# Kernel tuning notes

Measured on AMD Instinct MI355X. Metric: run time of the kernel, lower is better.

The kernel has to match this reference:

```python
import jax, jax.numpy as jnp
import numpy as np

B, S, D_IN, D_QK, D_V = 4, 4096, 1024, 64, 64

def setup_inputs() -> dict:
    key = jax.random.key(0)
    ks = jax.random.split(key, 8)
    sd = 1.0 / np.sqrt(D_IN)
    return {
        "X": jax.random.normal(ks[0], (B, S, D_IN), dtype=jnp.float32),
        "mask": jnp.ones((B, S, 1), dtype=jnp.float32),
        "Wq": jax.random.uniform(ks[1], (D_IN, D_QK), jnp.float32, -sd, sd),
        "bq": jax.random.uniform(ks[2], (D_QK,), jnp.float32, -sd, sd),
        "Wk": jax.random.uniform(ks[3], (D_IN, D_QK), jnp.float32, -sd, sd),
        "bk": jax.random.uniform(ks[4], (D_QK,), jnp.float32, -sd, sd),
        "Wv": jax.random.uniform(ks[5], (D_IN, D_V), jnp.float32, -sd, sd),
        "bv": jax.random.uniform(ks[6], (D_V,), jnp.float32, -sd, sd),
    }

def reference(X, mask, Wq, bq, Wk, bk, Wv, bv):
    # ReLU-activated projections (no head split, no 1/sqrt(d) scaling)
    q = jax.nn.relu(jnp.einsum('bsd,df->bsf', X, Wq) + bq)   # [B,S,D_QK]
    k = jax.nn.relu(jnp.einsum('bsd,df->bsf', X, Wk) + bk)   # [B,S,D_QK]
    v = jax.nn.relu(jnp.einsum('bsd,df->bsf', X, Wv) + bv)   # [B,S,D_V]
    scores = jax.nn.softmax(jnp.einsum('bqf,bkf->bqk', q, k), axis=-1)  # [B,S,S]
    return jnp.einsum('bqk,bkf->bqf', scores, v) * mask       # mask applied AFTER AV
```

## Files before the change

kernel.cpp:

```cpp
#include <hip/hip_runtime.h>


typedef short s16x8 __attribute__((ext_vector_type(8)));
typedef float fx4   __attribute__((ext_vector_type(4)));
typedef unsigned short u16x4 __attribute__((ext_vector_type(4)));

#define LOG2E 1.4426950408889634f

__device__ __forceinline__ unsigned short f2bf(float x) {
    unsigned int u = __float_as_uint(x);
    u += 0x7FFFu + ((u >> 16) & 1u);
    return (unsigned short)(u >> 16);
}
__device__ __forceinline__ float bf2f(unsigned short b) {
    return __uint_as_float(((unsigned int)b) << 16);
}

__global__ __launch_bounds__(256) void prep_w_kernel(
    const float* __restrict__ Wq, const float* __restrict__ Wk, const float* __restrict__ Wv,
    unsigned short* __restrict__ wt_hi, unsigned short* __restrict__ wt_lo)
{
    __shared__ __align__(16) unsigned short sh[64][72];
    __shared__ __align__(16) unsigned short sl[64][72];

    const int y  = blockIdx.x;
    const int kt = blockIdx.y;
    const float* W = (y == 0) ? Wq : (y == 1) ? Wk : Wv;
    const int t  = threadIdx.x;

    const int kl = t >> 2;
    const int c0 = (t & 3) * 16;
    const float* src = W + (size_t)(kt * 64 + kl) * 64 + c0;
    #pragma unroll
    for (int j = 0; j < 4; j++) {
        fx4 v = *(const fx4*)(src + j * 4);
        #pragma unroll
        for (int i = 0; i < 4; i++) {
            float x = v[i];
            unsigned short h = f2bf(x);
            unsigned short l = f2bf(x - bf2f(h));
            sh[c0 + j * 4 + i][kl] = h;
            sl[c0 + j * 4 + i][kl] = l;
        }
    }
    __syncthreads();

    const int c  = t >> 2;
    const int k0 = (t & 3) * 16;
    size_t o = (size_t)(y * 64 + c) * 1024 + kt * 64 + k0;
    *(s16x8*)(wt_hi + o)     = *(const s16x8*)&sh[c][k0];
    *(s16x8*)(wt_hi + o + 8) = *(const s16x8*)&sh[c][k0 + 8];
    *(s16x8*)(wt_lo + o)     = *(const s16x8*)&sl[c][k0];
    *(s16x8*)(wt_lo + o + 8) = *(const s16x8*)&sl[c][k0 + 8];
}

__global__ __launch_bounds__(768, 3) void proj_kernel(
    const float* __restrict__ X,
    const unsigned short* __restrict__ wt_hi, const unsigned short* __restrict__ wt_lo,
    const float* __restrict__ bq, const float* __restrict__ bk, const float* __restrict__ bv,
    unsigned short* __restrict__ q_hi, unsigned short* __restrict__ q_lo,
    unsigned short* __restrict__ k_bf, unsigned short* __restrict__ vt_g)
{
    __shared__ __align__(16) unsigned short a_hi[64][72];
    __shared__ __align__(16) unsigned short a_lo[64][72];
    __shared__ __align__(16) unsigned short bsh[192][72];
    __shared__ __align__(16) unsigned short bsl[192][72];

    const int tid  = threadIdx.x;
    const int lane = tid & 63;
    const int w    = tid >> 6;
    const int quad = lane >> 4;
    const int l15  = lane & 15;
    const int rowg = w & 1;
    const int colg = w >> 1;
    const int y    = colg >> 1;
    const int ch   = colg & 1;

    const int m0 = blockIdx.x * 64;

    fx4 acc[2][2];
    #pragma unroll
    for (int i = 0; i < 2; i++)
        #pragma unroll
        for (int j = 0; j < 2; j++) acc[i][j] = (fx4){0.f, 0.f, 0.f, 0.f};

    const int xrow = tid >> 4;
    const int xoff = (tid & 15) * 4;
    const float* xb0 = X + (size_t)(m0 + xrow) * 1024 + xoff;
    const float* xb1 = X + (size_t)(m0 + xrow + 32) * 1024 + xoff;

    const int wrow = tid >> 2;
    const int wk   = (tid & 3) * 16;
    const size_t wb = (size_t)wrow * 1024 + wk;

    fx4   xr[4][2];
    s16x8 wrh[2][2], wrl[2][2];
    if (tid < 512) {
        #pragma unroll
        for (int d = 0; d < 4; d++) {
            xr[d][0] = *(const fx4*)(xb0 + d * 64);
            xr[d][1] = *(const fx4*)(xb1 + d * 64);
        }
    }
    #pragma unroll
    for (int d = 0; d < 2; d++) {
        wrh[d][0] = *(const s16x8*)(wt_hi + wb + d * 64);
        wrh[d][1] = *(const s16x8*)(wt_hi + wb + d * 64 + 8);
        wrl[d][0] = *(const s16x8*)(wt_lo + wb + d * 64);
        wrl[d][1] = *(const s16x8*)(wt_lo + wb + d * 64 + 8);
    }

    #pragma unroll 4
    for (int kc = 0; kc < 16; kc++) {
        if (kc) __syncthreads();
        if (tid < 512) {
            #pragma unroll
            for (int i = 0; i < 2; i++) {
                fx4 xv = xr[kc & 3][i];
                unsigned short h0 = f2bf(xv.x), h1 = f2bf(xv.y), h2 = f2bf(xv.z), h3 = f2bf(xv.w);
                unsigned short l0 = f2bf(xv.x - bf2f(h0)), l1 = f2bf(xv.y - bf2f(h1));
                unsigned short l2 = f2bf(xv.z - bf2f(h2)), l3 = f2bf(xv.w - bf2f(h3));
                *(u16x4*)&a_hi[xrow + i * 32][xoff] = (u16x4){h0, h1, h2, h3};
                *(u16x4*)&a_lo[xrow + i * 32][xoff] = (u16x4){l0, l1, l2, l3};
            }
        }
        *(s16x8*)&bsh[wrow][wk]     = wrh[kc & 1][0];
        *(s16x8*)&bsh[wrow][wk + 8] = wrh[kc & 1][1];
        *(s16x8*)&bsl[wrow][wk]     = wrl[kc & 1][0];
        *(s16x8*)&bsl[wrow][wk + 8] = wrl[kc & 1][1];
        __syncthreads();

        if (tid < 512 && kc < 12) {
            xr[kc & 3][0] = *(const fx4*)(xb0 + (kc + 4) * 64);
            xr[kc & 3][1] = *(const fx4*)(xb1 + (kc + 4) * 64);
        }
        if (kc < 14) {
            wrh[kc & 1][0] = *(const s16x8*)(wt_hi + wb + (kc + 2) * 64);
            wrh[kc & 1][1] = *(const s16x8*)(wt_hi + wb + (kc + 2) * 64 + 8);
            wrl[kc & 1][0] = *(const s16x8*)(wt_lo + wb + (kc + 2) * 64);
            wrl[kc & 1][1] = *(const s16x8*)(wt_lo + wb + (kc + 2) * 64 + 8);
        }

        s16x8 ah[2][2], al[2][2];
        #pragma unroll
        for (int sub = 0; sub < 2; sub++)
            #pragma unroll
            for (int ks = 0; ks < 2; ks++) {
                const int r = rowg * 32 + sub * 16 + l15;
                ah[sub][ks] = *(const s16x8*)&a_hi[r][ks * 32 + quad * 8];
                al[sub][ks] = *(const s16x8*)&a_lo[r][ks * 32 + quad * 8];
            }
        #pragma unroll
        for (int nt = 0; nt < 2; nt++) {
            const int br = colg * 32 + nt * 16 + l15;
            #pragma unroll
            for (int ks = 0; ks < 2; ks++) {
                s16x8 bh = *(const s16x8*)&bsh[br][ks * 32 + quad * 8];
                s16x8 bl = *(const s16x8*)&bsl[br][ks * 32 + quad * 8];
                #pragma unroll
                for (int sub = 0; sub < 2; sub++) {
                    acc[sub][nt] = __builtin_amdgcn_mfma_f32_16x16x32_bf16(ah[sub][ks], bh, acc[sub][nt], 0, 0, 0);
                    acc[sub][nt] = __builtin_amdgcn_mfma_f32_16x16x32_bf16(ah[sub][ks], bl, acc[sub][nt], 0, 0, 0);
                    acc[sub][nt] = __builtin_amdgcn_mfma_f32_16x16x32_bf16(al[sub][ks], bh, acc[sub][nt], 0, 0, 0);
                }
            }
        }
    }
    __syncthreads();

    const float* bias = (y == 0) ? bq : (y == 1) ? bk : bv;
    const int b   = m0 >> 12;
    const int s0b = m0 & 4095;
    unsigned short* vtr = &a_hi[0][0];

    #pragma unroll
    for (int sub = 0; sub < 2; sub++)
        #pragma unroll
        for (int nt = 0; nt < 2; nt++) {
            const int col = ch * 32 + nt * 16 + l15;
            const float bb = bias[col];
            const int rloc = rowg * 32 + sub * 16 + quad * 4;
            #pragma unroll
            for (int r = 0; r < 4; r++) {
                float v = fmaxf(acc[sub][nt][r] + bb, 0.f);
                size_t grow = (size_t)(m0 + rloc + r);
                if (y == 0) {
                    unsigned short h = f2bf(v);
                    unsigned short l = f2bf(v - bf2f(h));
                    q_hi[grow * 64 + col] = h;
                    q_lo[grow * 64 + col] = l;
                } else if (y == 1) {
                    k_bf[grow * 64 + col] = f2bf(v);
                } else {
                    vtr[col * 72 + rloc + r] = f2bf(v);
                }
            }
        }
    __syncthreads();
    if (tid < 512) {
        int row = tid >> 3;
        int off = (tid & 7) * 8;
        s16x8 vv = *(const s16x8*)&vtr[row * 72 + off];
        *(s16x8*)(vt_g + (size_t)(b * 64 + row) * 4096 + s0b + off) = vv;
    }
}

__global__ __launch_bounds__(512, 2) void attn_kernel(
    const unsigned short* __restrict__ q_hi, const unsigned short* __restrict__ q_lo,
    const unsigned short* __restrict__ k_bf, const unsigned short* __restrict__ vt_g,
    unsigned short* __restrict__ pOb, float* __restrict__ pL)
{
    __shared__ __align__(16) unsigned short kt[128][72];
    __shared__ __align__(16) unsigned short vt[64][136];
    __shared__ __align__(16) unsigned short pt[8][32][40];

    const int tid  = threadIdx.x;
    const int lane = tid & 63;
    const int w    = tid >> 6;
    const int quad = lane >> 4;
    const int l15  = lane & 15;
    const int ck   = blockIdx.y;
    const int b    = blockIdx.z;
    const int q0   = blockIdx.x * 256;

    const size_t qbase = ((size_t)b * 4096 + q0 + w * 32 + l15) * 64 + quad * 8;
    s16x8 qh[2][2], ql[2][2];
    #pragma unroll
    for (int sub = 0; sub < 2; sub++) {
        qh[sub][0] = *(const s16x8*)(q_hi + qbase + sub * 1024);
        qh[sub][1] = *(const s16x8*)(q_hi + qbase + sub * 1024 + 32);
        ql[sub][0] = *(const s16x8*)(q_lo + qbase + sub * 1024);
        ql[sub][1] = *(const s16x8*)(q_lo + qbase + sub * 1024 + 32);
    }

    fx4 accO[2][4];
    #pragma unroll
    for (int sub = 0; sub < 2; sub++)
        #pragma unroll
        for (int nt = 0; nt < 4; nt++) accO[sub][nt] = (fx4){0.f, 0.f, 0.f, 0.f};
    float lsum[2][4] = {{0.f, 0.f, 0.f, 0.f}, {0.f, 0.f, 0.f, 0.f}};

    const unsigned short* kgb = k_bf + (size_t)b * 4096 * 64;
    const unsigned short* vgb = vt_g + (size_t)b * 64 * 4096;

    const int srow = tid >> 3;
    const int koff = (tid & 7) * 8;

    const unsigned short* kp = kgb + (size_t)(ck * 512) * 64;
    const unsigned short* vp = vgb + ck * 512;

    s16x8 nk0 = *(const s16x8*)(kp + (size_t)srow * 64 + koff);
    s16x8 nk1 = *(const s16x8*)(kp + (size_t)(srow + 64) * 64 + koff);
    s16x8 nv0 = *(const s16x8*)(vp + (size_t)srow * 4096 + koff);
    s16x8 nv1 = *(const s16x8*)(vp + (size_t)srow * 4096 + koff + 64);

    for (int t = 0; t < 4; t++) {
        *(s16x8*)&kt[srow][koff]      = nk0;
        *(s16x8*)&kt[srow + 64][koff] = nk1;
        *(s16x8*)&vt[srow][koff]      = nv0;
        *(s16x8*)&vt[srow][koff + 64] = nv1;
        __syncthreads();
        if (t < 3) {
            nk0 = *(const s16x8*)(kp + (size_t)(t + 1) * 8192 + (size_t)srow * 64 + koff);
            nk1 = *(const s16x8*)(kp + (size_t)(t + 1) * 8192 + (size_t)(srow + 64) * 64 + koff);
            nv0 = *(const s16x8*)(vp + (t + 1) * 128 + (size_t)srow * 4096 + koff);
            nv1 = *(const s16x8*)(vp + (t + 1) * 128 + (size_t)srow * 4096 + koff + 64);
        }

        #pragma unroll
        for (int h = 0; h < 2; h++) {
            #pragma unroll
            for (int kh = 0; kh < 2; kh++) {
                #pragma unroll
                for (int nt2 = 0; nt2 < 2; nt2++) {
                    const int key = h * 64 + kh * 32 + nt2 * 16 + l15;
                    s16x8 k0 = *(const s16x8*)&kt[key][quad * 8];
                    s16x8 k1 = *(const s16x8*)&kt[key][32 + quad * 8];
                    #pragma unroll
                    for (int sub = 0; sub < 2; sub++) {
                        fx4 sc = (fx4){0.f, 0.f, 0.f, 0.f};
                        __builtin_amdgcn_s_setprio(1);
                        sc = __builtin_amdgcn_mfma_f32_16x16x32_bf16(qh[sub][0], k0, sc, 0, 0, 0);
                        sc = __builtin_amdgcn_mfma_f32_16x16x32_bf16(ql[sub][0], k0, sc, 0, 0, 0);
                        sc = __builtin_amdgcn_mfma_f32_16x16x32_bf16(qh[sub][1], k1, sc, 0, 0, 0);
                        sc = __builtin_amdgcn_mfma_f32_16x16x32_bf16(ql[sub][1], k1, sc, 0, 0, 0);
                        __builtin_amdgcn_s_setprio(0);
                        #pragma unroll
                        for (int r = 0; r < 4; r++) {
                            float p = __builtin_amdgcn_exp2f(sc[r] * LOG2E);
                            unsigned short pb = f2bf(p);
                            lsum[sub][r] += bf2f(pb);
                            pt[w][sub * 16 + quad * 4 + r][nt2 * 16 + l15] = pb;
                        }
                    }
                }
                s16x8 pa0 = *(const s16x8*)&pt[w][l15][quad * 8];
                s16x8 pa1 = *(const s16x8*)&pt[w][16 + l15][quad * 8];
                __builtin_amdgcn_s_setprio(1);
                #pragma unroll
                for (int nt = 0; nt < 4; nt++) {
                    s16x8 vf = *(const s16x8*)&vt[nt * 16 + l15][h * 64 + kh * 32 + quad * 8];
                    accO[0][nt] = __builtin_amdgcn_mfma_f32_16x16x32_bf16(pa0, vf, accO[0][nt], 0, 0, 0);
                    accO[1][nt] = __builtin_amdgcn_mfma_f32_16x16x32_bf16(pa1, vf, accO[1][nt], 0, 0, 0);
                }
                __builtin_amdgcn_s_setprio(0);
            }
        }
        __syncthreads();
    }

    #pragma unroll
    for (int sub = 0; sub < 2; sub++)
        #pragma unroll
        for (int r = 0; r < 4; r++) {
            float v = lsum[sub][r];
            #pragma unroll
            for (int o = 1; o < 16; o <<= 1) v += __shfl_xor(v, o);
            lsum[sub][r] = v;
        }
    #pragma unroll
    for (int sub = 0; sub < 2; sub++)
        #pragma unroll
        for (int r = 0; r < 4; r++) {
            int qrow = q0 + w * 32 + sub * 16 + quad * 4 + r;
            size_t grow = (size_t)b * 4096 + qrow;
            #pragma unroll
            for (int nt = 0; nt < 4; nt++)
                pOb[((size_t)ck * 16384 + grow) * 64 + nt * 16 + l15] = f2bf(accO[sub][nt][r]);
            if (l15 == 0)
                pL[(size_t)ck * 16384 + grow] = lsum[sub][r];
        }
}

__global__ __launch_bounds__(256) void combine_kernel(
    const unsigned short* __restrict__ pOb, const float* __restrict__ pL,
    const float* __restrict__ mask, float* __restrict__ out)
{
    int idx = blockIdx.x * 256 + threadIdx.x;
    int q  = idx >> 4;
    int dg = idx & 15;
    fx4 s = (fx4){0.f, 0.f, 0.f, 0.f};
    float l = 0.f;
    #pragma unroll
    for (int c = 0; c < 8; c++) {
        u16x4 h = *(const u16x4*)(pOb + ((size_t)c * 16384 + q) * 64 + dg * 4);
        s.x += bf2f(h.x);
        s.y += bf2f(h.y);
        s.z += bf2f(h.z);
        s.w += bf2f(h.w);
        l += pL[(size_t)c * 16384 + q];
    }
    float scale = mask[q] / l;
    *(fx4*)(out + (size_t)q * 64 + dg * 4) = s * scale;
}

extern "C" void kernel_launch(void* const* d_in, const int* in_sizes, int n_in,
                              void* d_out, int out_size, void* d_ws, size_t ws_size,
                              hipStream_t stream)
{
    const float* X    = (const float*)d_in[0];
    const float* mask = (const float*)d_in[1];
    const float* Wq   = (const float*)d_in[2];
    const float* bq   = (const float*)d_in[3];
    const float* Wk   = (const float*)d_in[4];
    const float* bk   = (const float*)d_in[5];
    const float* Wv   = (const float*)d_in[6];
    const float* bv   = (const float*)d_in[7];
    float* out = (float*)d_out;

    char* ws = (char*)d_ws;
    unsigned short* q_hi  = (unsigned short*)(ws);
    unsigned short* q_lo  = (unsigned short*)(ws + (size_t)(2u << 20));
    unsigned short* k_bf  = (unsigned short*)(ws + (size_t)(4u << 20));
    unsigned short* vt_g  = (unsigned short*)(ws + (size_t)(6u << 20));
    unsigned short* wt_hi = (unsigned short*)(ws + (size_t)(8u << 20));
    unsigned short* wt_lo = (unsigned short*)(ws + (size_t)(8u << 20) + 393216);
    unsigned short* pOb   = (unsigned short*)(ws + (size_t)(9u << 20));
    float*          pL    = (float*)(ws + (size_t)(25u << 20));

    hipLaunchKernelGGL(prep_w_kernel, dim3(3, 16), dim3(256), 0, stream,
                       Wq, Wk, Wv, wt_hi, wt_lo);
    hipLaunchKernelGGL(proj_kernel, dim3(256), dim3(768), 0, stream,
                       X, wt_hi, wt_lo, bq, bk, bv, q_hi, q_lo, k_bf, vt_g);
    hipLaunchKernelGGL(attn_kernel, dim3(16, 8, 4), dim3(512), 0, stream,
                       q_hi, q_lo, k_bf, vt_g, pOb, pL);
    hipLaunchKernelGGL(combine_kernel, dim3(1024), dim3(256), 0, stream,
                       pOb, pL, mask, out);
}
```

Before: 162.4 us.

## Process two K-chunks per barrier in projection with XOR-swizzled LDS tiles

The projection GEMM now stages two 64-wide K chunks per iteration into double-sized shared buffers, which halves the number of __syncthreads pairs. The padded LDS rows (72 elements) are replaced by unpadded 64-element rows with an XOR swizzle on 8-element groups to avoid bank conflicts. Together these are meant to reduce barrier stalls and LDS padding. In exchange, LDS usage roughly doubles, which may limit occupancy at 768 threads with 3 blocks per CU, and the vtr alias in the epilogue now points at the first swizzled buffer.

```diff
diff --git a/kernel.cpp b/kernel.cpp
--- a/kernel.cpp
+++ b/kernel.cpp
@@ -61,10 +61,10 @@
     unsigned short* __restrict__ q_hi, unsigned short* __restrict__ q_lo,
     unsigned short* __restrict__ k_bf, unsigned short* __restrict__ vt_g)
 {
-    __shared__ __align__(16) unsigned short a_hi[64][72];
-    __shared__ __align__(16) unsigned short a_lo[64][72];
-    __shared__ __align__(16) unsigned short bsh[192][72];
-    __shared__ __align__(16) unsigned short bsl[192][72];
+    __shared__ __align__(16) unsigned short a_hi[2][64][64];
+    __shared__ __align__(16) unsigned short a_lo[2][64][64];
+    __shared__ __align__(16) unsigned short bsh[2][192][64];
+    __shared__ __align__(16) unsigned short bsl[2][192][64];
 
     const int tid  = threadIdx.x;
     const int lane = tid & 63;
@@ -92,6 +92,8 @@
     const int wrow = tid >> 2;
     const int wk   = (tid & 3) * 16;
     const size_t wb = (size_t)wrow * 1024 + wk;
+    const int wsw0 = (((wk >> 3)     ^ (wrow & 7)) << 3);
+    const int wsw1 = ((((wk >> 3) + 1) ^ (wrow & 7)) << 3);
 
     fx4   xr[4][2];
     s16x8 wrh[2][2], wrl[2][2];
@@ -110,58 +112,79 @@
         wrl[d][1] = *(const s16x8*)(wt_lo + wb + d * 64 + 8);
     }
 
-    #pragma unroll 4
-    for (int kc = 0; kc < 16; kc++) {
-        if (kc) __syncthreads();
-        if (tid < 512) {
-            #pragma unroll
-            for (int i = 0; i < 2; i++) {
-                fx4 xv = xr[kc & 3][i];
-                unsigned short h0 = f2bf(xv.x), h1 = f2bf(xv.y), h2 = f2bf(xv.z), h3 = f2bf(xv.w);
-                unsigned short l0 = f2bf(xv.x - bf2f(h0)), l1 = f2bf(xv.y - bf2f(h1));
-                unsigned short l2 = f2bf(xv.z - bf2f(h2)), l3 = f2bf(xv.w - bf2f(h3));
-                *(u16x4*)&a_hi[xrow + i * 32][xoff] = (u16x4){h0, h1, h2, h3};
-                *(u16x4*)&a_lo[xrow + i * 32][xoff] = (u16x4){l0, l1, l2, l3};
-            }
-        }
-        *(s16x8*)&bsh[wrow][wk]     = wrh[kc & 1][0];
-        *(s16x8*)&bsh[wrow][wk + 8] = wrh[kc & 1][1];
-        *(s16x8*)&bsl[wrow][wk]     = wrl[kc & 1][0];
-        *(s16x8*)&bsl[wrow][wk + 8] = wrl[kc & 1][1];
+    #pragma unroll 2
+    for (int ph = 0; ph < 8; ph++) {
+        if (ph) __syncthreads();
+        #pragma unroll
+        for (int half = 0; half < 2; half++) {
+            const int kc = 2 * ph + half;
+            if (tid < 512) {
+                #pragma unroll
+                for (int i = 0; i < 2; i++) {
+                    fx4 xv = xr[kc & 3][i];
+                    unsigned short h0 = f2bf(xv.x), h1 = f2bf(xv.y), h2 = f2bf(xv.z), h3 = f2bf(xv.w);
+                    unsigned short l0 = f2bf(xv.x - bf2f(h0)), l1 = f2bf(xv.y - bf2f(h1));
+                    unsigned short l2 = f2bf(xv.z - bf2f(h2)), l3 = f2bf(xv.w - bf2f(h3));
+                    const int row = xrow + i * 32;
+                    const int sw  = ((((xoff >> 3) ^ (row & 7)) << 3) | (xoff & 7));
+                    *(u16x4*)&a_hi[half][row][sw] = (u16x4){h0, h1, h2, h3};
+                    *(u16x4*)&a_lo[half][row][sw] = (u16x4){l0, l1, l2, l3};
+                }
+            }
+            *(s16x8*)&bsh[half][wrow][wsw0] = wrh[half][0];
+            *(s16x8*)&bsh[half][wrow][wsw1] = wrh[half][1];
+            *(s16x8*)&bsl[half][wrow][wsw0] = wrl[half][0];
+            *(s16x8*)&bsl[half][wrow][wsw1] = wrl[half][1];
+        }
         __syncthreads();
 
-        if (tid < 512 && kc < 12) {
-            xr[kc & 3][0] = *(const fx4*)(xb0 + (kc + 4) * 64);
-            xr[kc & 3][1] = *(const fx4*)(xb1 + (kc + 4) * 64);
-        }
-        if (kc < 14) {
-            wrh[kc & 1][0] = *(const s16x8*)(wt_hi + wb + (kc + 2) * 64);
-            wrh[kc & 1][1] = *(const s16x8*)(wt_hi + wb + (kc + 2) * 64 + 8);
-            wrl[kc & 1][0] = *(const s16x8*)(wt_lo + wb + (kc + 2) * 64);
-            wrl[kc & 1][1] = *(const s16x8*)(wt_lo + wb + (kc + 2) * 64 + 8);
-        }
-
-        s16x8 ah[2][2], al[2][2];
-        #pragma unroll
-        for (int sub = 0; sub < 2; sub++)
-            #pragma unroll
-            for (int ks = 0; ks < 2; ks++) {
-                const int r = rowg * 32 + sub * 16 + l15;
-                ah[sub][ks] = *(const s16x8*)&a_hi[r][ks * 32 + quad * 8];
-                al[sub][ks] = *(const s16x8*)&a_lo[r][ks * 32 + quad * 8];
-            }
-        #pragma unroll
-        for (int nt = 0; nt < 2; nt++) {
-            const int br = colg * 32 + nt * 16 + l15;
-            #pragma unroll
-            for (int ks = 0; ks < 2; ks++) {
-                s16x8 bh = *(const s16x8*)&bsh[br][ks * 32 + quad * 8];
-                s16x8 bl = *(const s16x8*)&bsl[br][ks * 32 + quad * 8];
+        if (tid < 512 && ph < 6) {
+            #pragma unroll
+            for (int half = 0; half < 2; half++) {
+                const int kc = 2 * ph + 4 + half;
+                xr[kc & 3][0] = *(const fx4*)(xb0 + kc * 64);
+                xr[kc & 3][1] = *(const fx4*)(xb1 + kc * 64);
+            }
+        }
+        if (ph < 7) {
+            #pragma unroll
+            for (int half = 0; half < 2; half++) {
+                const int kc = 2 * ph + 2 + half;
+                wrh[half][0] = *(const s16x8*)(wt_hi + wb + kc * 64);
+                wrh[half][1] = *(const s16x8*)(wt_hi + wb + kc * 64 + 8);
+                wrl[half][0] = *(const s16x8*)(wt_lo + wb + kc * 64);
+                wrl[half][1] = *(const s16x8*)(wt_lo + wb + kc * 64 + 8);
+            }
+        }
+
+        #pragma unroll
+        for (int half = 0; half < 2; half++) {
+            const int r = rowg * 32 + (  0) * 16 + l15;
+            s16x8 ah[2][2], al[2][2];
+            #pragma unroll
+            for (int sub = 0; sub < 2; sub++)
                 #pragma unroll
-                for (int sub = 0; sub < 2; sub++) {
-                    acc[sub][nt] = __builtin_amdgcn_mfma_f32_16x16x32_bf16(ah[sub][ks], bh, acc[sub][nt], 0, 0, 0);
-                    acc[sub][nt] = __builtin_amdgcn_mfma_f32_16x16x32_bf16(ah[sub][ks], bl, acc[sub][nt], 0, 0, 0);
-                    acc[sub][nt] = __builtin_amdgcn_mfma_f32_16x16x32_bf16(al[sub][ks], bh, acc[sub][nt], 0, 0, 0);
+                for (int ks = 0; ks < 2; ks++) {
+                    const int rr = rowg * 32 + sub * 16 + l15;
+                    const int sw = (((ks * 4 + quad) ^ (rr & 7)) << 3);
+                    ah[sub][ks] = *(const s16x8*)&a_hi[half][rr][sw];
+                    al[sub][ks] = *(const s16x8*)&a_lo[half][rr][sw];
+                }
+            (void)r;
+            #pragma unroll
+            for (int nt = 0; nt < 2; nt++) {
+                const int br = colg * 32 + nt * 16 + l15;
+                #pragma unroll
+                for (int ks = 0; ks < 2; ks++) {
+                    const int sw = (((ks * 4 + quad) ^ (br & 7)) << 3);
+                    s16x8 bh = *(const s16x8*)&bsh[half][br][sw];
+                    s16x8 bl = *(const s16x8*)&bsl[half][br][sw];
+                    #pragma unroll
+                    for (int sub = 0; sub < 2; sub++) {
+                        acc[sub][nt] = __builtin_amdgcn_mfma_f32_16x16x32_bf16(ah[sub][ks], bh, acc[sub][nt], 0, 0, 0);
+                        acc[sub][nt] = __builtin_amdgcn_mfma_f32_16x16x32_bf16(ah[sub][ks], bl, acc[sub][nt], 0, 0, 0);
+                        acc[sub][nt] = __builtin_amdgcn_mfma_f32_16x16x32_bf16(al[sub][ks], bh, acc[sub][nt], 0, 0, 0);
+                    }
                 }
             }
         }
@@ -171,7 +194,7 @@
     const float* bias = (y == 0) ? bq : (y == 1) ? bk : bv;
     const int b   = m0 >> 12;
     const int s0b = m0 & 4095;
-    unsigned short* vtr = &a_hi[0][0];
+    unsigned short* vtr = &a_hi[0][0][0];
 
     #pragma unroll
     for (int sub = 0; sub < 2; sub++)
```

New measurement: 160.9 us. About the same (-0.9%).

## Halve projection row tile, swizzle LDS tiles, and deepen weight prefetch

Applied to the files above, without the earlier changes.

The projection kernel now handles 32 rows per block with 6 waves, one per 32-column group, instead of 64 rows with 12 waves. It launches twice as many blocks (512), which fills more CUs on the GPU. Unpadded LDS tiles use an XOR swizzle to avoid bank conflicts, and each thread loads wider 32-element weight chunks one stage ahead. The trade-off is that each weight tile is reused across fewer rows, so total weight traffic from L2 doubles.

```diff
diff --git a/kernel.cpp b/kernel.cpp
--- a/kernel.cpp
+++ b/kernel.cpp
@@ -54,29 +54,28 @@
     *(s16x8*)(wt_lo + o + 8) = *(const s16x8*)&sl[c][k0 + 8];
 }
 
-__global__ __launch_bounds__(768, 3) void proj_kernel(
+__global__ __launch_bounds__(384, 3) void proj_kernel(
     const float* __restrict__ X,
     const unsigned short* __restrict__ wt_hi, const unsigned short* __restrict__ wt_lo,
     const float* __restrict__ bq, const float* __restrict__ bk, const float* __restrict__ bv,
     unsigned short* __restrict__ q_hi, unsigned short* __restrict__ q_lo,
     unsigned short* __restrict__ k_bf, unsigned short* __restrict__ vt_g)
 {
-    __shared__ __align__(16) unsigned short a_hi[64][72];
-    __shared__ __align__(16) unsigned short a_lo[64][72];
-    __shared__ __align__(16) unsigned short bsh[192][72];
-    __shared__ __align__(16) unsigned short bsl[192][72];
+    __shared__ __align__(16) unsigned short a_hi[32][64];
+    __shared__ __align__(16) unsigned short a_lo[32][64];
+    __shared__ __align__(16) unsigned short bsh[192][64];
+    __shared__ __align__(16) unsigned short bsl[192][64];
 
     const int tid  = threadIdx.x;
     const int lane = tid & 63;
     const int w    = tid >> 6;
     const int quad = lane >> 4;
     const int l15  = lane & 15;
-    const int rowg = w & 1;
-    const int colg = w >> 1;
+    const int colg = w;
     const int y    = colg >> 1;
     const int ch   = colg & 1;
 
-    const int m0 = blockIdx.x * 64;
+    const int m0 = blockIdx.x * 32;
 
     fx4 acc[2][2];
     #pragma unroll
@@ -84,61 +83,65 @@
         #pragma unroll
         for (int j = 0; j < 2; j++) acc[i][j] = (fx4){0.f, 0.f, 0.f, 0.f};
 
-    const int xrow = tid >> 4;
-    const int xoff = (tid & 15) * 4;
-    const float* xb0 = X + (size_t)(m0 + xrow) * 1024 + xoff;
-    const float* xb1 = X + (size_t)(m0 + xrow + 32) * 1024 + xoff;
-
-    const int wrow = tid >> 2;
-    const int wk   = (tid & 3) * 16;
+    const int xrow = tid >> 3;
+    const int xch  = tid & 7;
+    const float* xb = X + (size_t)(m0 + xrow) * 1024 + xch * 8;
+    const int xsw  = ((xch ^ (xrow & 7)) << 3);
+
+    const int wrow = tid >> 1;
+    const int wk   = (tid & 1) * 32;
     const size_t wb = (size_t)wrow * 1024 + wk;
 
     fx4   xr[4][2];
-    s16x8 wrh[2][2], wrl[2][2];
-    if (tid < 512) {
+    s16x8 wrh[4], wrl[4];
+    if (tid < 256) {
         #pragma unroll
         for (int d = 0; d < 4; d++) {
-            xr[d][0] = *(const fx4*)(xb0 + d * 64);
-            xr[d][1] = *(const fx4*)(xb1 + d * 64);
-        }
-    }
-    #pragma unroll
-    for (int d = 0; d < 2; d++) {
-        wrh[d][0] = *(const s16x8*)(wt_hi + wb + d * 64);
-        wrh[d][1] = *(const s16x8*)(wt_hi + wb + d * 64 + 8);
-        wrl[d][0] = *(const s16x8*)(wt_lo + wb + d * 64);
-        wrl[d][1] = *(const s16x8*)(wt_lo + wb + d * 64 + 8);
+            xr[d][0] = *(const fx4*)(xb + d * 64);
+            xr[d][1] = *(const fx4*)(xb + d * 64 + 4);
+        }
+    }
+    #pragma unroll
+    for (int j = 0; j < 4; j++) {
+        wrh[j] = *(const s16x8*)(wt_hi + wb + j * 8);
+        wrl[j] = *(const s16x8*)(wt_lo + wb + j * 8);
     }
 
     #pragma unroll 4
     for (int kc = 0; kc < 16; kc++) {
         if (kc) __syncthreads();
-        if (tid < 512) {
-            #pragma unroll
-            for (int i = 0; i < 2; i++) {
-                fx4 xv = xr[kc & 3][i];
-                unsigned short h0 = f2bf(xv.x), h1 = f2bf(xv.y), h2 = f2bf(xv.z), h3 = f2bf(xv.w);
-                unsigned short l0 = f2bf(xv.x - bf2f(h0)), l1 = f2bf(xv.y - bf2f(h1));
-                unsigned short l2 = f2bf(xv.z - bf2f(h2)), l3 = f2bf(xv.w - bf2f(h3));
-                *(u16x4*)&a_hi[xrow + i * 32][xoff] = (u16x4){h0, h1, h2, h3};
-                *(u16x4*)&a_lo[xrow + i * 32][xoff] = (u16x4){l0, l1, l2, l3};
-            }
-        }
-        *(s16x8*)&bsh[wrow][wk]     = wrh[kc & 1][0];
-        *(s16x8*)&bsh[wrow][wk + 8] = wrh[kc & 1][1];
-        *(s16x8*)&bsl[wrow][wk]     = wrl[kc & 1][0];
-        *(s16x8*)&bsl[wrow][wk + 8] = wrl[kc & 1][1];
+        if (tid < 256) {
+            fx4 xa = xr[kc & 3][0], xb2 = xr[kc & 3][1];
+            unsigned short h0 = f2bf(xa.x), h1 = f2bf(xa.y), h2 = f2bf(xa.z), h3 = f2bf(xa.w);
+            unsigned short h4 = f2bf(xb2.x), h5 = f2bf(xb2.y), h6 = f2bf(xb2.z), h7 = f2bf(xb2.w);
+            unsigned short l0 = f2bf(xa.x - bf2f(h0)), l1 = f2bf(xa.y - bf2f(h1));
+            unsigned short l2 = f2bf(xa.z - bf2f(h2)), l3 = f2bf(xa.w - bf2f(h3));
+            unsigned short l4 = f2bf(xb2.x - bf2f(h4)), l5 = f2bf(xb2.y - bf2f(h5));
+            unsigned short l6 = f2bf(xb2.z - bf2f(h6)), l7 = f2bf(xb2.w - bf2f(h7));
+            *(u16x4*)&a_hi[xrow][xsw]     = (u16x4){h0, h1, h2, h3};
+            *(u16x4*)&a_hi[xrow][xsw + 4] = (u16x4){h4, h5, h6, h7};
+            *(u16x4*)&a_lo[xrow][xsw]     = (u16x4){l0, l1, l2, l3};
+            *(u16x4*)&a_lo[xrow][xsw + 4] = (u16x4){l4, l5, l6, l7};
+        }
+        #pragma unroll
+        for (int j = 0; j < 4; j++) {
+            const int cj = (wk >> 3) + j;
+            const int sw = ((cj ^ (wrow & 7)) << 3);
+            *(s16x8*)&bsh[wrow][sw] = wrh[j];
+            *(s16x8*)&bsl[wrow][sw] = wrl[j];
+        }
         __syncthreads();
 
-        if (tid < 512 && kc < 12) {
-            xr[kc & 3][0] = *(const fx4*)(xb0 + (kc + 4) * 64);
-            xr[kc & 3][1] = *(const fx4*)(xb1 + (kc + 4) * 64);
-        }
-        if (kc < 14) {
-            wrh[kc & 1][0] = *(const s16x8*)(wt_hi + wb + (kc + 2) * 64);
-            wrh[kc & 1][1] = *(const s16x8*)(wt_hi + wb + (kc + 2) * 64 + 8);
-            wrl[kc & 1][0] = *(const s16x8*)(wt_lo + wb + (kc + 2) * 64);
-            wrl[kc & 1][1] = *(const s16x8*)(wt_lo + wb + (kc + 2) * 64 + 8);
+        if (tid < 256 && kc < 12) {
+            xr[kc & 3][0] = *(const fx4*)(xb + (kc + 4) * 64);
+            xr[kc & 3][1] = *(const fx4*)(xb + (kc + 4) * 64 + 4);
+        }
+        if (kc < 15) {
+            #pragma unroll
+            for (int j = 0; j < 4; j++) {
+                wrh[j] = *(const s16x8*)(wt_hi + wb + (kc + 1) * 64 + j * 8);
+                wrl[j] = *(const s16x8*)(wt_lo + wb + (kc + 1) * 64 + j * 8);
+            }
         }
 
         s16x8 ah[2][2], al[2][2];
@@ -146,17 +149,19 @@
         for (int sub = 0; sub < 2; sub++)
             #pragma unroll
             for (int ks = 0; ks < 2; ks++) {
-                const int r = rowg * 32 + sub * 16 + l15;
-                ah[sub][ks] = *(const s16x8*)&a_hi[r][ks * 32 + quad * 8];
-                al[sub][ks] = *(const s16x8*)&a_lo[r][ks * 32 + quad * 8];
+                const int rr = sub * 16 + l15;
+                const int sw = (((ks * 4 + quad) ^ (rr & 7)) << 3);
+                ah[sub][ks] = *(const s16x8*)&a_hi[rr][sw];
+                al[sub][ks] = *(const s16x8*)&a_lo[rr][sw];
             }
         #pragma unroll
         for (int nt = 0; nt < 2; nt++) {
             const int br = colg * 32 + nt * 16 + l15;
             #pragma unroll
             for (int ks = 0; ks < 2; ks++) {
-                s16x8 bh = *(const s16x8*)&bsh[br][ks * 32 + quad * 8];
-                s16x8 bl = *(const s16x8*)&bsl[br][ks * 32 + quad * 8];
+                const int sw = (((ks * 4 + quad) ^ (br & 7)) << 3);
+                s16x8 bh = *(const s16x8*)&bsh[br][sw];
+                s16x8 bl = *(const s16x8*)&bsl[br][sw];
                 #pragma unroll
                 for (int sub = 0; sub < 2; sub++) {
                     acc[sub][nt] = __builtin_amdgcn_mfma_f32_16x16x32_bf16(ah[sub][ks], bh, acc[sub][nt], 0, 0, 0);
@@ -171,7 +176,7 @@
     const float* bias = (y == 0) ? bq : (y == 1) ? bk : bv;
     const int b   = m0 >> 12;
     const int s0b = m0 & 4095;
-    unsigned short* vtr = &a_hi[0][0];
+    unsigned short* vtr = &bsh[0][0];
 
     #pragma unroll
     for (int sub = 0; sub < 2; sub++)
@@ -179,7 +184,7 @@
         for (int nt = 0; nt < 2; nt++) {
             const int col = ch * 32 + nt * 16 + l15;
             const float bb = bias[col];
-            const int rloc = rowg * 32 + sub * 16 + quad * 4;
+            const int rloc = sub * 16 + quad * 4;
             #pragma unroll
             for (int r = 0; r < 4; r++) {
                 float v = fmaxf(acc[sub][nt][r] + bb, 0.f);
@@ -192,15 +197,15 @@
                 } else if (y == 1) {
                     k_bf[grow * 64 + col] = f2bf(v);
                 } else {
-                    vtr[col * 72 + rloc + r] = f2bf(v);
+                    vtr[col * 48 + rloc + r] = f2bf(v);
                 }
             }
         }
     __syncthreads();
-    if (tid < 512) {
-        int row = tid >> 3;
-        int off = (tid & 7) * 8;
-        s16x8 vv = *(const s16x8*)&vtr[row * 72 + off];
+    if (tid < 256) {
+        int row = tid >> 2;
+        int off = (tid & 3) * 8;
+        s16x8 vv = *(const s16x8*)&vtr[row * 48 + off];
         *(s16x8*)(vt_g + (size_t)(b * 64 + row) * 4096 + s0b + off) = vv;
     }
 }
@@ -380,7 +385,7 @@
 
     hipLaunchKernelGGL(prep_w_kernel, dim3(3, 16), dim3(256), 0, stream,
                        Wq, Wk, Wv, wt_hi, wt_lo);
-    hipLaunchKernelGGL(proj_kernel, dim3(256), dim3(768), 0, stream,
+    hipLaunchKernelGGL(proj_kernel, dim3(512), dim3(384), 0, stream,
                        X, wt_hi, wt_lo, bq, bk, bv, q_hi, q_lo, k_bf, vt_g);
     hipLaunchKernelGGL(attn_kernel, dim3(16, 8, 4), dim3(512), 0, stream,
                        q_hi, q_lo, k_bf, vt_g, pOb, pL);
```

Measured after the change: 182.3 us. 1.12x slower.
